# Kernel tuning notes

Hardware: AMD Instinct MI355X
Metric: run time of the kernel (lower is better)

The kernel has to match this reference:

```python
import jax, jax.numpy as jnp
import numpy as np

E, T_MAX, H, L, V = 384, 256, 6, 6, 65
DH = E // H  # 64
EPS = 1e-5


def setup_inputs() -> dict:
    key = jax.random.key(0)
    ks = jax.random.split(key, 24)
    B, T = 128, 256
    s = 0.02
    inp = {
        "input_indices": jax.random.randint(ks[0], (B, T), 0, V, dtype=jnp.int64) if jax.config.read("jax_enable_x64") else jax.random.randint(ks[0], (B, T), 0, V, dtype=jnp.int32),
        "targets": jax.random.randint(ks[1], (B, T), 0, V, dtype=jnp.int32),
        "tok_emb": s * jax.random.normal(ks[2], (V, E), jnp.float32),
        "pos_emb": s * jax.random.normal(ks[3], (T_MAX, E), jnp.float32),
        "Wq": s * jax.random.normal(ks[4], (L, H, E, DH), jnp.float32),
        "Wk": s * jax.random.normal(ks[5], (L, H, E, DH), jnp.float32),
        "Wv": s * jax.random.normal(ks[6], (L, H, E, DH), jnp.float32),
        "Wo": s * jax.random.normal(ks[7], (L, E, E), jnp.float32),
        "bo": jnp.zeros((L, E), jnp.float32),
        "ln1_s": jnp.ones((L, E), jnp.float32),
        "ln1_b": jnp.zeros((L, E), jnp.float32),
        "ln2_s": jnp.ones((L, E), jnp.float32),
        "ln2_b": jnp.zeros((L, E), jnp.float32),
        "W1": s * jax.random.normal(ks[8], (L, E, 4 * E), jnp.float32),
        "b1": jnp.zeros((L, 4 * E), jnp.float32),
        "W2": s * jax.random.normal(ks[9], (L, 4 * E, E), jnp.float32),
        "b2": jnp.zeros((L, E), jnp.float32),
        "lnf_s": jnp.ones((E,), jnp.float32),
        "lnf_b": jnp.zeros((E,), jnp.float32),
        "Wout": s * jax.random.normal(ks[10], (E, V), jnp.float32),
        "bout": jnp.zeros((V,), jnp.float32),
    }
    return inp


def _ln(x, s, b):
    m = x.mean(-1, keepdims=True)
    v = ((x - m) ** 2).mean(-1, keepdims=True)
    return (x - m) * jax.lax.rsqrt(v + EPS) * s + b


def _forward(input_indices, targets, tok_emb, pos_emb, Wq, Wk, Wv, Wo, bo,
             ln1_s, ln1_b, ln2_s, ln2_b, W1, b1, W2, b2, lnf_s, lnf_b, Wout, bout):
    B, T = input_indices.shape
    x = tok_emb[input_indices] + pos_emb[:T]  # [B,T,E]
    causal = jnp.tril(jnp.ones((T, T), bool))
    scale = DH ** -0.5

    def block(x, p):
        wq, wk, wv, wo, bo_, l1s, l1b, l2s, l2b, w1, b1_, w2, b2_ = p
        h = _ln(x, l1s, l1b)
        q = jnp.einsum("bte,hed->bhtd", h, wq)
        k = jnp.einsum("bte,hed->bhtd", h, wk)
        v = jnp.einsum("bte,hed->bhtd", h, wv)
        scores = jnp.einsum("bhtd,bhsd->bhts", q, k) * scale
        scores = jnp.where(causal, scores, -jnp.inf)
        w = jax.nn.softmax(scores, axis=-1)
        att = jnp.einsum("bhts,bhsd->bhtd", w, v)  # [B,H,T,DH]
        att = att.transpose(0, 2, 1, 3).reshape(B, T, E)  # concat heads
        x = x + att @ wo + bo_
        h2 = _ln(x, l2s, l2b)
        ff = jax.nn.relu(h2 @ w1 + b1_) @ w2 + b2_
        return x + ff, None

    x, _ = jax.lax.scan(block, x, (Wq, Wk, Wv, Wo, bo, ln1_s, ln1_b, ln2_s, ln2_b, W1, b1, W2, b2))
    x = _ln(x, lnf_s, lnf_b)
    logits = x @ Wout + bout  # [B,T,V]
    logp = jax.nn.log_softmax(logits, axis=-1)
    nll = -jnp.take_along_axis(logp, targets[..., None], axis=-1)[..., 0]
    loss = nll.mean()
    return logits, loss


def reference(input_indices, targets, tok_emb, pos_emb, Wq, Wk, Wv, Wo, bo,
              ln1_s, ln1_b, ln2_s, ln2_b, W1, b1, W2, b2, lnf_s, lnf_b, Wout, bout):
    return _forward(input_indices, targets, tok_emb, pos_emb, Wq, Wk, Wv, Wo, bo,
                    ln1_s, ln1_b, ln2_s, ln2_b, W1, b1, W2, b2, lnf_s, lnf_b, Wout, bout)
```

## Files before the change

### kernel.cpp

```cpp
#include <hip/hip_runtime.h>

#define BT      32768
#define T_SEQ   256
#define E_DIM   384
#define NH      6
#define NL      6
#define VOC     65
#define FF_DIM  1536
#define QKV_N   1152

typedef short bf16x8 __attribute__((ext_vector_type(8)));
typedef float f32x4  __attribute__((ext_vector_type(4)));
typedef unsigned short u16;

typedef const unsigned int __attribute__((address_space(1))) gu32;
typedef unsigned int       __attribute__((address_space(3))) lu32;

__device__ __forceinline__ u16 f2bf(float x) {
  unsigned u = __builtin_bit_cast(unsigned, x);
  u += 0x7fffu + ((u >> 16) & 1u);
  return (u16)(u >> 16);
}
__device__ __forceinline__ float bf2f(u16 v) {
  unsigned u = ((unsigned)v) << 16;
  return __builtin_bit_cast(float, u);
}

__device__ __forceinline__ void load_lds_16(const void* g, void* l) {
  __builtin_amdgcn_global_load_lds((gu32*)g, (lu32*)l, 16, 0, 0);
}

__global__ __launch_bounds__(256) void transpose_t(
    const float* __restrict__ src, u16* __restrict__ dst, int R, int C,
    long sbs, long dbs_outer, int inner, long dbs_inner, long dbase) {
  __shared__ float t[32][33];
  const int b = blockIdx.z;
  const float* s = src + (long)b * sbs;
  u16* d = dst + dbase + (long)(b / inner) * dbs_outer + (long)(b % inner) * dbs_inner;
  const int r0 = blockIdx.x * 32, c0 = blockIdx.y * 32;
  const int tx = threadIdx.x & 31, ty = threadIdx.x >> 5;
#pragma unroll
  for (int i = 0; i < 4; i++) {
    int rr = ty + i * 8;
    int r = r0 + rr, c = c0 + tx;
    if (r < R && c < C) t[rr][tx] = s[(long)r * C + c];
  }
  __syncthreads();
#pragma unroll
  for (int i = 0; i < 4; i++) {
    int cc = ty + i * 8;
    int c = c0 + cc, r = r0 + tx;
    if (c < C && r < R) d[(long)c * R + r] = f2bf(t[tx][cc]);
  }
}

__global__ __launch_bounds__(256) void embed_k(const int* __restrict__ idx,
                                               const float* __restrict__ tok,
                                               const float* __restrict__ pos,
                                               u16* __restrict__ x) {
  int i = blockIdx.x * 256 + threadIdx.x;
  int bt = i / 48, q = i - bt * 48;
  int t = bt & 255;
  const float4* tp = (const float4*)(tok + (size_t)idx[bt] * E_DIM + q * 8);
  const float4* pp = (const float4*)(pos + (size_t)t * E_DIM + q * 8);
  float4 a0 = tp[0], a1 = tp[1], p0 = pp[0], p1 = pp[1];
  u16 o[8];
  o[0] = f2bf(a0.x + p0.x); o[1] = f2bf(a0.y + p0.y);
  o[2] = f2bf(a0.z + p0.z); o[3] = f2bf(a0.w + p0.w);
  o[4] = f2bf(a1.x + p1.x); o[5] = f2bf(a1.y + p1.y);
  o[6] = f2bf(a1.z + p1.z); o[7] = f2bf(a1.w + p1.w);
  *(bf16x8*)(x + (size_t)bt * E_DIM + q * 8) = *(bf16x8*)o;
}

__global__ __launch_bounds__(256) void ln_k(const u16* __restrict__ x,
                                            const float* __restrict__ gam,
                                            const float* __restrict__ bet,
                                            u16* __restrict__ out) {
  int tid = threadIdx.x, lane = tid & 63, w = tid >> 6;
  size_t token = (size_t)blockIdx.x * 4 + w;
  const u16* xr = x + token * E_DIM;
  u16 raw[6];
  *(uint2*)raw          = *(const uint2*)(xr + 4 * lane);
  *(unsigned*)(raw + 4) = *(const unsigned*)(xr + 256 + 2 * lane);
  float v[6]; float s = 0.f;
#pragma unroll
  for (int i = 0; i < 6; i++) { v[i] = bf2f(raw[i]); s += v[i]; }
#pragma unroll
  for (int d = 1; d < 64; d <<= 1) s += __shfl_xor(s, d);
  float mean = s * (1.f / E_DIM);
  float q = 0.f;
#pragma unroll
  for (int i = 0; i < 6; i++) { float d0 = v[i] - mean; q += d0 * d0; }
#pragma unroll
  for (int d = 1; d < 64; d <<= 1) q += __shfl_xor(q, d);
  float r = rsqrtf(q * (1.f / E_DIM) + 1e-5f);
  int e[6] = {4 * lane, 4 * lane + 1, 4 * lane + 2, 4 * lane + 3,
              256 + 2 * lane, 256 + 2 * lane + 1};
  u16 o[6];
#pragma unroll
  for (int i = 0; i < 6; i++)
    o[i] = f2bf((v[i] - mean) * r * gam[e[i]] + bet[e[i]]);
  u16* orow = out + token * E_DIM;
  *(uint2*)(orow + 4 * lane)          = *(uint2*)o;
  *(unsigned*)(orow + 256 + 2 * lane) = *(unsigned*)(o + 4);
}

__global__ __launch_bounds__(256) void gemm_d(
    const u16* __restrict__ A, const u16* __restrict__ Bt, int K, int Nstore,
    const float* __restrict__ bias, const u16* __restrict__ resid,
    u16* __restrict__ outH, float* __restrict__ outF, int relu) {
  __shared__ u16 smem[16384];
  u16* As = smem;
  u16* Bs = smem + 8192;
  const int tid = threadIdx.x, lane = tid & 63, wv = tid >> 6;
  const int quad = lane >> 4, l16 = lane & 15;
  const int m0 = blockIdx.x * 128, n0 = blockIdx.y * 128;
  const int wm = (wv & 1) * 64, wn = (wv >> 1) * 64;

  const int lrow = lane >> 2;
  const int lchunk = (lane & 3) ^ ((lane >> 3) & 3);

  f32x4 acc[4][4];
#pragma unroll
  for (int i = 0; i < 4; i++)
#pragma unroll
    for (int j = 0; j < 4; j++) acc[i][j] = (f32x4){0.f, 0.f, 0.f, 0.f};

  auto stage = [&](int sel, int k0) {
#pragma unroll
    for (int j = 0; j < 2; j++) {
      int rid = wv * 2 + j;
      int r = rid * 16 + lrow;
      load_lds_16(A + (size_t)(m0 + r) * K + k0 + lchunk * 8, &As[sel * 4096 + rid * 512]);
      load_lds_16(Bt + (size_t)(n0 + r) * K + k0 + lchunk * 8, &Bs[sel * 4096 + rid * 512]);
    }
  };

  const int NK = K >> 5;
  stage(0, 0);
  __syncthreads();
  const int slot = (quad ^ ((l16 >> 1) & 3)) * 8;
  for (int kt = 0; kt < NK; kt++) {
    const int cur = kt & 1;
    if (kt + 1 < NK) stage(cur ^ 1, (kt + 1) * 32);
    const u16* Ab = As + cur * 4096;
    const u16* Bb = Bs + cur * 4096;
    bf16x8 af[4], bfr[4];
#pragma unroll
    for (int i = 0; i < 4; i++) af[i]  = *(const bf16x8*)&Ab[(wm + i * 16 + l16) * 32 + slot];
#pragma unroll
    for (int j = 0; j < 4; j++) bfr[j] = *(const bf16x8*)&Bb[(wn + j * 16 + l16) * 32 + slot];
#pragma unroll
    for (int i = 0; i < 4; i++)
#pragma unroll
      for (int j = 0; j < 4; j++)
        acc[i][j] = __builtin_amdgcn_mfma_f32_16x16x32_bf16(af[i], bfr[j], acc[i][j], 0, 0, 0);
    __syncthreads();
  }

  if (outH) {
#pragma unroll
    for (int p = 0; p < 4; p++) {
      if (p) __syncthreads();
      if ((wv >> 1) == (p >> 1)) {
#pragma unroll
        for (int jj = 0; jj < 2; jj++) {
          int j = (p & 1) * 2 + jj;
          int gn = n0 + wn + j * 16 + l16;
          float bv = bias ? bias[gn] : 0.f;
          int lcol = jj * 16 + l16;
#pragma unroll
          for (int i = 0; i < 4; i++)
#pragma unroll
            for (int r = 0; r < 4; r++) {
              float v = acc[i][j][r] + bv;
              if (relu) v = fmaxf(v, 0.f);
              smem[(wm + i * 16 + quad * 4 + r) * 36 + lcol] = f2bf(v);
            }
        }
      }
      __syncthreads();
      const int gc0 = n0 + p * 32;
#pragma unroll
      for (int s = 0; s < 4; s++) {
        int row = s * 32 + (tid >> 3);
        int seg = (tid & 7) * 4;
        u16 pk[4];
        *(uint2*)pk = *(const uint2*)&smem[row * 36 + seg];
        size_t o = (size_t)(m0 + row) * Nstore + gc0 + seg;
        if (resid) {
          u16 rv[4];
          *(uint2*)rv = *(const uint2*)&resid[o];
#pragma unroll
          for (int q2 = 0; q2 < 4; q2++) pk[q2] = f2bf(bf2f(pk[q2]) + bf2f(rv[q2]));
        }
        *(uint2*)&outH[o] = *(uint2*)pk;
      }
    }
  } else {
#pragma unroll
    for (int j = 0; j < 4; j++) {
      const int gn = n0 + wn + j * 16 + l16;
      if (gn < Nstore) {
        const float bv = bias ? bias[gn] : 0.f;
#pragma unroll
        for (int i = 0; i < 4; i++)
#pragma unroll
          for (int r = 0; r < 4; r++) {
            const int gm = m0 + wm + i * 16 + quad * 4 + r;
            outF[(size_t)gm * Nstore + gn] = acc[i][j][r] + bv;
          }
      }
    }
  }
}

__global__ __launch_bounds__(512, 2) void ffn_k(
    const u16* __restrict__ hb, const u16* __restrict__ W1t,
    const float* __restrict__ b1, const u16* __restrict__ W2t,
    const float* __restrict__ b2, u16* __restrict__ x) {
  __shared__ __align__(16) u16 sm[73728];
  u16* As = sm;
  u16* Ps = sm + 49152;
  const int tid = threadIdx.x, lane = tid & 63, w = tid >> 6;
  const int quad = lane >> 4, l16 = lane & 15;
  const int wm  = (w >> 2) * 64;
  const int wn1 = (w & 3) * 48;
  const int wn2 = (w & 3) * 96;
  const int m0 = blockIdx.x * 128;
  const int lrow = lane >> 2;
  const int lchunk = (lane & 3) ^ ((lane >> 3) & 3);
  const int slot = (quad ^ ((l16 >> 1) & 3)) * 8;

#pragma unroll
  for (int p = 0; p < 12; p++)
    load_lds_16(hb + (size_t)(m0 + w * 16 + lrow) * E_DIM + p * 32 + lchunk * 8,
                &As[p * 4096 + w * 512]);

  f32x4 oacc[4][6];
#pragma unroll
  for (int i = 0; i < 4; i++)
#pragma unroll
    for (int o = 0; o < 6; o++) oacc[i][o] = (f32x4){0.f, 0.f, 0.f, 0.f};

  __syncthreads();

  for (int j = 0; j < 8; j++) {
    const int jb = j * 192;
    f32x4 pacc[4][3];
#pragma unroll
    for (int i = 0; i < 4; i++)
#pragma unroll
      for (int f = 0; f < 3; f++) pacc[i][f] = (f32x4){0.f, 0.f, 0.f, 0.f};
    for (int ks = 0; ks < 12; ks++) {
      bf16x8 af[4], wf[3];
#pragma unroll
      for (int f = 0; f < 3; f++)
        wf[f] = *(const bf16x8*)(W1t + (size_t)(jb + wn1 + f * 16 + l16) * E_DIM +
                                 ks * 32 + quad * 8);
#pragma unroll
      for (int i = 0; i < 4; i++)
        af[i] = *(const bf16x8*)&As[ks * 4096 + (wm + i * 16 + l16) * 32 + slot];
#pragma unroll
      for (int i = 0; i < 4; i++)
#pragma unroll
        for (int f = 0; f < 3; f++)
          pacc[i][f] = __builtin_amdgcn_mfma_f32_16x16x32_bf16(af[i], wf[f], pacc[i][f], 0, 0, 0);
    }
    float bv[3];
#pragma unroll
    for (int f = 0; f < 3; f++) bv[f] = b1[jb + wn1 + f * 16 + l16];
#pragma unroll
    for (int i = 0; i < 4; i++)
#pragma unroll
      for (int f = 0; f < 3; f++) {
        const int colb = wn1 + f * 16 + l16;
        const int ch = colb >> 3;
#pragma unroll
        for (int r = 0; r < 4; r++) {
          const int row = wm + i * 16 + quad * 4 + r;
          Ps[row * 192 + (ch ^ (row & 7)) * 8 + (colb & 7)] =
              f2bf(fmaxf(pacc[i][f][r] + bv[f], 0.f));
        }
      }
    __syncthreads();
    for (int ks = 0; ks < 6; ks++) {
      bf16x8 pf[4], bfr[6];
#pragma unroll
      for (int o = 0; o < 6; o++)
        bfr[o] = *(const bf16x8*)(W2t + (size_t)(wn2 + o * 16 + l16) * FF_DIM +
                                  jb + ks * 32 + quad * 8);
#pragma unroll
      for (int i = 0; i < 4; i++) {
        const int row = wm + i * 16 + l16;
        pf[i] = *(const bf16x8*)&Ps[row * 192 + ((ks * 4 + quad) ^ (row & 7)) * 8];
      }
#pragma unroll
      for (int i = 0; i < 4; i++)
#pragma unroll
        for (int o = 0; o < 6; o++)
          oacc[i][o] = __builtin_amdgcn_mfma_f32_16x16x32_bf16(pf[i], bfr[o], oacc[i][o], 0, 0, 0);
    }
    __syncthreads();
  }

  float bv2[6];
#pragma unroll
  for (int o = 0; o < 6; o++) bv2[o] = b2[wn2 + o * 16 + l16];
#pragma unroll
  for (int i = 0; i < 4; i++)
#pragma unroll
    for (int o = 0; o < 6; o++) {
      const int col = wn2 + o * 16 + l16;
#pragma unroll
      for (int r = 0; r < 4; r++) {
        const int row = wm + i * 16 + quad * 4 + r;
        sm[row * 392 + col] = f2bf(oacc[i][o][r] + bv2[o]);
      }
    }
  __syncthreads();
  const int er = tid >> 3, ec = tid & 7;
#pragma unroll
  for (int rh = 0; rh < 2; rh++)
#pragma unroll
    for (int seg = 0; seg < 6; seg++) {
      const int row = rh * 64 + er;
      const int col = (seg * 8 + ec) * 8;
      u16 pk[8];
      *(uint4*)pk = *(const uint4*)&sm[row * 392 + col];
      const size_t g = (size_t)(m0 + row) * E_DIM + col;
      uint4 rv4 = *(const uint4*)&x[g];
      const u16* rv = (const u16*)&rv4;
#pragma unroll
      for (int q2 = 0; q2 < 8; q2++) pk[q2] = f2bf(bf2f(pk[q2]) + bf2f(rv[q2]));
      *(uint4*)&x[g] = *(uint4*)pk;
    }
}

__global__ __launch_bounds__(512) void attn_k(const u16* __restrict__ qkv,
                                              u16* __restrict__ att) {
  __shared__ u16 Kc[64 * 64];
  __shared__ u16 Vtc[64 * 64];
  __shared__ u16 Pl[8 * 16 * 64];
  const int b = blockIdx.x / NH, h = blockIdx.x % NH;
  const int tid = threadIdx.x, lane = tid & 63, w = tid >> 6;
  const int quad = lane >> 4, l16 = lane & 15;
  const int rowb = b * T_SEQ;
  const int tiles[2] = {w, 15 - w};

  bf16x8 qf[2][2];
#pragma unroll
  for (int ti = 0; ti < 2; ti++)
#pragma unroll
    for (int kk = 0; kk < 2; kk++)
      qf[ti][kk] = *(const bf16x8*)(qkv + (size_t)(rowb + tiles[ti] * 16 + l16) * QKV_N +
                                    h * 64 + kk * 32 + quad * 8);

  f32x4 Oa[2][4];
  float mrun[2][4], lrun[2][4];
#pragma unroll
  for (int ti = 0; ti < 2; ti++) {
#pragma unroll
    for (int di = 0; di < 4; di++) Oa[ti][di] = (f32x4){0.f, 0.f, 0.f, 0.f};
#pragma unroll
    for (int r = 0; r < 4; r++) { mrun[ti][r] = -1e30f; lrun[ti][r] = 0.f; }
  }

  u16* Pw = &Pl[w * 1024];
  const int sr = tid >> 3, sseg = tid & 7;
  const int kst = sseg ^ (sr & 7) ^ ((sr >> 3) & 7);

  for (int c = 0; c < 4; c++) {
    const int s0 = c * 64;
    __syncthreads();
    *(uint4*)&Kc[sr * 64 + kst * 8] =
        *(const uint4*)(qkv + (size_t)(rowb + s0 + sr) * QKV_N + 384 + h * 64 + sseg * 8);
    {
      union { uint4 u; u16 us[8]; } tb;
      tb.u = *(const uint4*)(qkv + (size_t)(rowb + s0 + sr) * QKV_N + 768 + h * 64 + sseg * 8);
#pragma unroll
      for (int j = 0; j < 8; j++) {
        int d = sseg * 8 + j;
        int vst = (sr >> 3) ^ (d & 7) ^ ((d >> 3) & 7);
        Vtc[d * 64 + vst * 8 + (sr & 7)] = tb.us[j];
      }
    }
    __syncthreads();

    bf16x8 kf[4][2], vf[4][2];
    bool loaded = false;
#pragma unroll
    for (int ti = 0; ti < 2; ti++) {
      const int t = tiles[ti];
      if (t < 4 * c) continue;
      if (!loaded) {
        loaded = true;
#pragma unroll
        for (int ni = 0; ni < 4; ni++)
#pragma unroll
          for (int kk = 0; kk < 2; kk++) {
            int srow = ni * 16 + l16;
            int ks = (kk * 4 + quad) ^ (srow & 7) ^ ((srow >> 3) & 7);
            kf[ni][kk] = *(const bf16x8*)&Kc[srow * 64 + ks * 8];
            int drow = ni * 16 + l16;
            int vs = (kk * 4 + quad) ^ (drow & 7) ^ ((drow >> 3) & 7);
            vf[ni][kk] = *(const bf16x8*)&Vtc[drow * 64 + vs * 8];
          }
      }
      f32x4 S[4];
#pragma unroll
      for (int ni = 0; ni < 4; ni++) {
        f32x4 z = (f32x4){0.f, 0.f, 0.f, 0.f};
        z = __builtin_amdgcn_mfma_f32_16x16x32_bf16(qf[ti][0], kf[ni][0], z, 0, 0, 0);
        S[ni] = __builtin_amdgcn_mfma_f32_16x16x32_bf16(qf[ti][1], kf[ni][1], z, 0, 0, 0);
      }
      const bool diag = ((t >> 2) == c);
#pragma unroll
      for (int ni = 0; ni < 4; ni++)
#pragma unroll
        for (int r = 0; r < 4; r++) {
          float xv = S[ni][r] * 0.125f;
          if (diag) {
            int trow = t * 16 + quad * 4 + r;
            int s = s0 + ni * 16 + l16;
            if (s > trow) xv = -1e30f;
          }
          S[ni][r] = xv;
        }
#pragma unroll
      for (int r = 0; r < 4; r++) {
        float mx = fmaxf(fmaxf(S[0][r], S[1][r]), fmaxf(S[2][r], S[3][r]));
        mx = fmaxf(mx, __shfl_xor(mx, 1));
        mx = fmaxf(mx, __shfl_xor(mx, 2));
        mx = fmaxf(mx, __shfl_xor(mx, 4));
        mx = fmaxf(mx, __shfl_xor(mx, 8));
        float mnew = fmaxf(mrun[ti][r], mx);
        float alpha = __expf(mrun[ti][r] - mnew);
        float ls = 0.f;
#pragma unroll
        for (int ni = 0; ni < 4; ni++) {
          float p = __expf(S[ni][r] - mnew);
          S[ni][r] = p; ls += p;
        }
        ls += __shfl_xor(ls, 1); ls += __shfl_xor(ls, 2);
        ls += __shfl_xor(ls, 4); ls += __shfl_xor(ls, 8);
        lrun[ti][r] = lrun[ti][r] * alpha + ls;
        mrun[ti][r] = mnew;
#pragma unroll
        for (int di = 0; di < 4; di++) Oa[ti][di][r] *= alpha;
      }
#pragma unroll
      for (int ni = 0; ni < 4; ni++)
#pragma unroll
        for (int r = 0; r < 4; r++) {
          int ch = 2 * ni + (l16 >> 3);
          int st = ch ^ (quad | ((r & 1) << 2));
          Pw[(quad * 4 + r) * 64 + st * 8 + (l16 & 7)] = f2bf(S[ni][r]);
        }
      bf16x8 pf[2];
#pragma unroll
      for (int kk = 0; kk < 2; kk++) {
        int key = (l16 >> 2) | ((l16 & 1) << 2);
        int st = (kk * 4 + quad) ^ key;
        pf[kk] = *(const bf16x8*)&Pw[l16 * 64 + st * 8];
      }
#pragma unroll
      for (int di = 0; di < 4; di++) {
        Oa[ti][di] = __builtin_amdgcn_mfma_f32_16x16x32_bf16(pf[0], vf[di][0], Oa[ti][di], 0, 0, 0);
        Oa[ti][di] = __builtin_amdgcn_mfma_f32_16x16x32_bf16(pf[1], vf[di][1], Oa[ti][di], 0, 0, 0);
      }
    }
  }

#pragma unroll
  for (int ti = 0; ti < 2; ti++)
#pragma unroll
    for (int r = 0; r < 4; r++) {
      float inv = 1.f / lrun[ti][r];
      int trow = tiles[ti] * 16 + quad * 4 + r;
#pragma unroll
      for (int di = 0; di < 4; di++)
        att[(size_t)(rowb + trow) * E_DIM + h * 64 + di * 16 + l16] = f2bf(Oa[ti][di][r] * inv);
    }
}

__global__ __launch_bounds__(256) void loss_k(const float* __restrict__ logits,
                                              const int* __restrict__ tgt,
                                              float* __restrict__ loss) {
  __shared__ float part[4];
  const int tid = threadIdx.x, lane = tid & 63, w = tid >> 6;
  const int wave_id = blockIdx.x * 4 + w;
  float acc = 0.f;
  for (int t = wave_id; t < BT; t += 2048) {
    const float* row = logits + (size_t)t * VOC;
    float a = row[lane];
    float b = (lane == 0) ? row[64] : -1e30f;
    float mx = fmaxf(a, b);
#pragma unroll
    for (int d = 1; d < 64; d <<= 1) mx = fmaxf(mx, __shfl_xor(mx, d));
    float sum = __expf(a - mx) + ((lane == 0) ? __expf(b - mx) : 0.f);
#pragma unroll
    for (int d = 1; d < 64; d <<= 1) sum += __shfl_xor(sum, d);
    if (lane == 0) acc += mx + __logf(sum) - row[tgt[t]];
  }
  if (lane == 0) part[w] = acc;
  __syncthreads();
  if (tid == 0)
    atomicAdd(loss, (part[0] + part[1] + part[2] + part[3]) * (1.f / (float)BT));
}

extern "C" void kernel_launch(void* const* d_in, const int* in_sizes, int n_in,
                              void* d_out, int out_size, void* d_ws, size_t ws_size,
                              hipStream_t stream) {
  (void)in_sizes; (void)n_in; (void)out_size; (void)ws_size;
  const int*   idx  = (const int*)d_in[0];
  const int*   tgt  = (const int*)d_in[1];
  const float* tok  = (const float*)d_in[2];
  const float* pos  = (const float*)d_in[3];
  const float* Wq   = (const float*)d_in[4];
  const float* Wk   = (const float*)d_in[5];
  const float* Wv   = (const float*)d_in[6];
  const float* Wo   = (const float*)d_in[7];
  const float* bo   = (const float*)d_in[8];
  const float* ln1s = (const float*)d_in[9];
  const float* ln1b = (const float*)d_in[10];
  const float* ln2s = (const float*)d_in[11];
  const float* ln2b = (const float*)d_in[12];
  const float* W1   = (const float*)d_in[13];
  const float* b1   = (const float*)d_in[14];
  const float* W2   = (const float*)d_in[15];
  const float* b2   = (const float*)d_in[16];
  const float* lnfs = (const float*)d_in[17];
  const float* lnfb = (const float*)d_in[18];
  const float* Wout = (const float*)d_in[19];
  const float* bout = (const float*)d_in[20];

  char* w = (char*)d_ws;
  u16* x      = (u16*)w;    w += (size_t)BT * E_DIM * 2;
  u16* hb     = (u16*)w;    w += (size_t)BT * E_DIM * 2;
  u16* attb   = (u16*)w;    w += (size_t)BT * E_DIM * 2;
  u16* big    = (u16*)w;    w += (size_t)BT * FF_DIM * 2;
  u16* Wqkv_t = (u16*)w;    w += (size_t)NL * QKV_N * E_DIM * 2;
  u16* Wo_t   = (u16*)w;    w += (size_t)NL * E_DIM * E_DIM * 2;
  u16* W1_t   = (u16*)w;    w += (size_t)NL * FF_DIM * E_DIM * 2;
  u16* W2_t   = (u16*)w;    w += (size_t)NL * E_DIM * FF_DIM * 2;
  u16* Wout_t = (u16*)w;    w += (size_t)128 * E_DIM * 2;
  u16* qkv = big;

  float* logits = (float*)d_out;
  float* loss   = logits + (size_t)BT * VOC;

  hipMemsetAsync(Wout_t, 0, 128 * E_DIM * 2, stream);
  transpose_t<<<dim3(12, 2, 36), 256, 0, stream>>>(Wq, Wqkv_t, 384, 64,
      24576, 442368, 6, 24576, 0);
  transpose_t<<<dim3(12, 2, 36), 256, 0, stream>>>(Wk, Wqkv_t, 384, 64,
      24576, 442368, 6, 24576, (long)384 * 384);
  transpose_t<<<dim3(12, 2, 36), 256, 0, stream>>>(Wv, Wqkv_t, 384, 64,
      24576, 442368, 6, 24576, (long)768 * 384);
  transpose_t<<<dim3(12, 12, 6), 256, 0, stream>>>(Wo, Wo_t, 384, 384,
      147456, 147456, 1, 0, 0);
  transpose_t<<<dim3(12, 48, 6), 256, 0, stream>>>(W1, W1_t, 384, 1536,
      589824, 589824, 1, 0, 0);
  transpose_t<<<dim3(48, 12, 6), 256, 0, stream>>>(W2, W2_t, 1536, 384,
      589824, 589824, 1, 0, 0);
  transpose_t<<<dim3(12, 3, 1), 256, 0, stream>>>(Wout, Wout_t, 384, 65,
      0, 0, 1, 0, 0);

  embed_k<<<6144, 256, 0, stream>>>(idx, tok, pos, x);

  for (int l = 0; l < NL; l++) {
    ln_k<<<8192, 256, 0, stream>>>(x, ln1s + l * E_DIM, ln1b + l * E_DIM, hb);
    gemm_d<<<dim3(256, 9), 256, 0, stream>>>(hb, Wqkv_t + (size_t)l * QKV_N * E_DIM,
                                             384, QKV_N, nullptr, nullptr, qkv, nullptr, 0);
    attn_k<<<768, 512, 0, stream>>>(qkv, attb);
    gemm_d<<<dim3(256, 3), 256, 0, stream>>>(attb, Wo_t + (size_t)l * E_DIM * E_DIM,
                                             384, E_DIM, bo + l * E_DIM, x, x, nullptr, 0);
    ln_k<<<8192, 256, 0, stream>>>(x, ln2s + l * E_DIM, ln2b + l * E_DIM, hb);
    ffn_k<<<256, 512, 0, stream>>>(hb, W1_t + (size_t)l * FF_DIM * E_DIM, b1 + l * FF_DIM,
                                   W2_t + (size_t)l * E_DIM * FF_DIM, b2 + l * E_DIM, x);
  }
  ln_k<<<8192, 256, 0, stream>>>(x, lnfs, lnfb, hb);
  gemm_d<<<dim3(256, 1), 256, 0, stream>>>(hb, Wout_t, 384, VOC, bout, nullptr, nullptr, logits, 0);

  hipMemsetAsync(loss, 0, 4, stream);
  loss_k<<<512, 256, 0, stream>>>(logits, tgt, loss);
}
```

Before: 2.099 ms.

## Halve FFN block tile to 64 rows and double-buffer weight fragments in registers

The fused FFN kernel now runs 256-thread blocks that each own 64 rows, launched as 512 blocks instead of 256 blocks of 512 threads over 128 rows. Shared memory per block halves. Both inner GEMM loops now use ping-pong register buffers so the next k-step's W1/W2 fragments are fetched from global memory while the current MFMAs execute. This targets global-load latency stalls and aims for better spreading of work across CUs. The cost is twice the total weight traffic, since each block re-reads the full W1/W2 for fewer rows, plus higher register pressure from the extra fragment buffers.

```diff
diff --git a/kernel.cpp b/kernel.cpp
--- a/kernel.cpp
+++ b/kernel.cpp
@@ -215,19 +215,18 @@
   }
 }
 
-__global__ __launch_bounds__(512, 2) void ffn_k(
+__global__ __launch_bounds__(256, 2) void ffn_k(
     const u16* __restrict__ hb, const u16* __restrict__ W1t,
     const float* __restrict__ b1, const u16* __restrict__ W2t,
     const float* __restrict__ b2, u16* __restrict__ x) {
-  __shared__ __align__(16) u16 sm[73728];
+  __shared__ __align__(16) u16 sm[36864];
   u16* As = sm;
-  u16* Ps = sm + 49152;
+  u16* Ps = sm + 24576;
   const int tid = threadIdx.x, lane = tid & 63, w = tid >> 6;
   const int quad = lane >> 4, l16 = lane & 15;
-  const int wm  = (w >> 2) * 64;
-  const int wn1 = (w & 3) * 48;
-  const int wn2 = (w & 3) * 96;
-  const int m0 = blockIdx.x * 128;
+  const int wn1 = w * 48;
+  const int wn2 = w * 96;
+  const int m0 = blockIdx.x * 64;
   const int lrow = lane >> 2;
   const int lchunk = (lane & 3) ^ ((lane >> 3) & 3);
   const int slot = (quad ^ ((l16 >> 1) & 3)) * 8;
@@ -235,7 +234,7 @@
 #pragma unroll
   for (int p = 0; p < 12; p++)
     load_lds_16(hb + (size_t)(m0 + w * 16 + lrow) * E_DIM + p * 32 + lchunk * 8,
-                &As[p * 4096 + w * 512]);
+                &As[p * 2048 + w * 512]);
 
   f32x4 oacc[4][6];
 #pragma unroll
@@ -247,25 +246,42 @@
 
   for (int j = 0; j < 8; j++) {
     const int jb = j * 192;
+    const u16* W1c = W1t + (size_t)(jb + wn1 + l16) * E_DIM;
     f32x4 pacc[4][3];
 #pragma unroll
     for (int i = 0; i < 4; i++)
 #pragma unroll
       for (int f = 0; f < 3; f++) pacc[i][f] = (f32x4){0.f, 0.f, 0.f, 0.f};
-    for (int ks = 0; ks < 12; ks++) {
-      bf16x8 af[4], wf[3];
+    bf16x8 wfA[3], wfB[3];
+#pragma unroll
+    for (int f = 0; f < 3; f++)
+      wfA[f] = *(const bf16x8*)(W1c + (size_t)f * 16 * E_DIM + quad * 8);
+#pragma unroll 1
+    for (int ks = 0; ks < 12; ks += 2) {
 #pragma unroll
       for (int f = 0; f < 3; f++)
-        wf[f] = *(const bf16x8*)(W1t + (size_t)(jb + wn1 + f * 16 + l16) * E_DIM +
-                                 ks * 32 + quad * 8);
+        wfB[f] = *(const bf16x8*)(W1c + (size_t)f * 16 * E_DIM + (ks + 1) * 32 + quad * 8);
+      bf16x8 af[4];
 #pragma unroll
       for (int i = 0; i < 4; i++)
-        af[i] = *(const bf16x8*)&As[ks * 4096 + (wm + i * 16 + l16) * 32 + slot];
+        af[i] = *(const bf16x8*)&As[ks * 2048 + (i * 16 + l16) * 32 + slot];
 #pragma unroll
       for (int i = 0; i < 4; i++)
 #pragma unroll
         for (int f = 0; f < 3; f++)
-          pacc[i][f] = __builtin_amdgcn_mfma_f32_16x16x32_bf16(af[i], wf[f], pacc[i][f], 0, 0, 0);
+          pacc[i][f] = __builtin_amdgcn_mfma_f32_16x16x32_bf16(af[i], wfA[f], pacc[i][f], 0, 0, 0);
+      if (ks < 10)
+#pragma unroll
+        for (int f = 0; f < 3; f++)
+          wfA[f] = *(const bf16x8*)(W1c + (size_t)f * 16 * E_DIM + (ks + 2) * 32 + quad * 8);
+#pragma unroll
+      for (int i = 0; i < 4; i++)
+        af[i] = *(const bf16x8*)&As[(ks + 1) * 2048 + (i * 16 + l16) * 32 + slot];
+#pragma unroll
+      for (int i = 0; i < 4; i++)
+#pragma unroll
+        for (int f = 0; f < 3; f++)
+          pacc[i][f] = __builtin_amdgcn_mfma_f32_16x16x32_bf16(af[i], wfB[f], pacc[i][f], 0, 0, 0);
     }
     float bv[3];
 #pragma unroll
@@ -278,28 +294,47 @@
         const int ch = colb >> 3;
 #pragma unroll
         for (int r = 0; r < 4; r++) {
-          const int row = wm + i * 16 + quad * 4 + r;
+          const int row = i * 16 + quad * 4 + r;
           Ps[row * 192 + (ch ^ (row & 7)) * 8 + (colb & 7)] =
               f2bf(fmaxf(pacc[i][f][r] + bv[f], 0.f));
         }
       }
     __syncthreads();
-    for (int ks = 0; ks < 6; ks++) {
-      bf16x8 pf[4], bfr[6];
+    const u16* W2c = W2t + (size_t)(wn2 + l16) * FF_DIM + jb;
+    bf16x8 bfA[6], bfB[6];
+#pragma unroll
+    for (int o = 0; o < 6; o++)
+      bfA[o] = *(const bf16x8*)(W2c + (size_t)o * 16 * FF_DIM + quad * 8);
+#pragma unroll 1
+    for (int ks = 0; ks < 6; ks += 2) {
 #pragma unroll
       for (int o = 0; o < 6; o++)
-        bfr[o] = *(const bf16x8*)(W2t + (size_t)(wn2 + o * 16 + l16) * FF_DIM +
-                                  jb + ks * 32 + quad * 8);
+        bfB[o] = *(const bf16x8*)(W2c + (size_t)o * 16 * FF_DIM + (ks + 1) * 32 + quad * 8);
+      bf16x8 pf[4];
 #pragma unroll
       for (int i = 0; i < 4; i++) {
-        const int row = wm + i * 16 + l16;
+        const int row = i * 16 + l16;
         pf[i] = *(const bf16x8*)&Ps[row * 192 + ((ks * 4 + quad) ^ (row & 7)) * 8];
       }
 #pragma unroll
       for (int i = 0; i < 4; i++)
 #pragma unroll
         for (int o = 0; o < 6; o++)
-          oacc[i][o] = __builtin_amdgcn_mfma_f32_16x16x32_bf16(pf[i], bfr[o], oacc[i][o], 0, 0, 0);
+          oacc[i][o] = __builtin_amdgcn_mfma_f32_16x16x32_bf16(pf[i], bfA[o], oacc[i][o], 0, 0, 0);
+      if (ks < 4)
+#pragma unroll
+        for (int o = 0; o < 6; o++)
+          bfA[o] = *(const bf16x8*)(W2c + (size_t)o * 16 * FF_DIM + (ks + 2) * 32 + quad * 8);
+#pragma unroll
+      for (int i = 0; i < 4; i++) {
+        const int row = i * 16 + l16;
+        pf[i] = *(const bf16x8*)&Ps[row * 192 + (((ks + 1) * 4 + quad) ^ (row & 7)) * 8];
+      }
+#pragma unroll
+      for (int i = 0; i < 4; i++)
+#pragma unroll
+        for (int o = 0; o < 6; o++)
+          oacc[i][o] = __builtin_amdgcn_mfma_f32_16x16x32_bf16(pf[i], bfB[o], oacc[i][o], 0, 0, 0);
     }
     __syncthreads();
   }
@@ -314,7 +349,7 @@
       const int col = wn2 + o * 16 + l16;
 #pragma unroll
       for (int r = 0; r < 4; r++) {
-        const int row = wm + i * 16 + quad * 4 + r;
+        const int row = i * 16 + quad * 4 + r;
         sm[row * 392 + col] = f2bf(oacc[i][o][r] + bv2[o]);
       }
     }
@@ -324,7 +359,7 @@
   for (int rh = 0; rh < 2; rh++)
 #pragma unroll
     for (int seg = 0; seg < 6; seg++) {
-      const int row = rh * 64 + er;
+      const int row = rh * 32 + er;
       const int col = (seg * 8 + ec) * 8;
       u16 pk[8];
       *(uint4*)pk = *(const uint4*)&sm[row * 392 + col];
@@ -576,7 +611,7 @@
     gemm_d<<<dim3(256, 3), 256, 0, stream>>>(attb, Wo_t + (size_t)l * E_DIM * E_DIM,
                                              384, E_DIM, bo + l * E_DIM, x, x, nullptr, 0);
     ln_k<<<8192, 256, 0, stream>>>(x, ln2s + l * E_DIM, ln2b + l * E_DIM, hb);
-    ffn_k<<<256, 512, 0, stream>>>(hb, W1_t + (size_t)l * FF_DIM * E_DIM, b1 + l * FF_DIM,
+    ffn_k<<<512, 256, 0, stream>>>(hb, W1_t + (size_t)l * FF_DIM * E_DIM, b1 + l * FF_DIM,
                                    W2_t + (size_t)l * E_DIM * FF_DIM, b2 + l * E_DIM, x);
   }
   ln_k<<<8192, 256, 0, stream>>>(x, lnfs, lnfb, hb);
```

Measured after the change: 1.919 ms. 8.6% less time.
